# Optimization experiments

Measured on AMD Instinct MI355X. Metric: run time of the kernel, lower is better.

The kernel has to match this reference:

```python
import jax, jax.numpy as jnp
import numpy as np

N = 50000   # num nodes
E = 800000  # num edges
D = 128     # in_features
C = 1.0     # curvature c
MIN_NORM = 1e-15
BALL_EPS = 4e-3  # float32 boundary eps in PoincareBall.proj


def setup_inputs() -> dict:
    key = jax.random.key(0)
    k1, k2 = jax.random.split(key)
    x = jax.random.normal(k1, (N, D), dtype=jnp.float32)
    edge_index = jax.random.randint(k2, (2, E), 0, N, dtype=jnp.int32)
    return {"x": x, "edge_index": edge_index}


def _expmap0(u, c):
    sqrt_c = c ** 0.5
    u_norm = jnp.maximum(jnp.linalg.norm(u, axis=-1, keepdims=True), MIN_NORM)
    return jnp.tanh(sqrt_c * u_norm) * u / (sqrt_c * u_norm)


def _proj(p, c):
    norm = jnp.maximum(jnp.linalg.norm(p, axis=-1, keepdims=True), MIN_NORM)
    maxnorm = (1.0 - BALL_EPS) / (c ** 0.5)
    return jnp.where(norm > maxnorm, p / norm * maxnorm, p)


def reference(x, edge_index):
    row, col = edge_index[0], edge_index[1]
    # add_remaining_self_loops: drop existing self-loops (weight->0), append N fresh self-loops w=1
    w = jnp.where(row == col, 0.0, 1.0).astype(x.dtype)
    loop = jnp.arange(N, dtype=row.dtype)
    row_f = jnp.concatenate([row, loop])
    col_f = jnp.concatenate([col, loop])
    w_f = jnp.concatenate([w, jnp.ones((N,), x.dtype)])
    # symmetric GCN normalization: D^{-1/2} A D^{-1/2}
    deg = jax.ops.segment_sum(w_f, row_f, num_segments=N)
    dis = jnp.where(deg > 0, 1.0 / jnp.sqrt(jnp.where(deg > 0, deg, 1.0)), 0.0)
    nw = dis[row_f] * w_f * dis[col_f]  # [E+N]
    # gather source features, weighted scatter-add into destination rows
    support = nw[:, None] * x[col_f]                       # [E+N, D]
    result = jax.ops.segment_sum(support, row_f, num_segments=N)  # [N, D]
    return _proj(_expmap0(result, C), C)
```

## Files before the change

### kernel.cpp

```cpp
#include <hip/hip_runtime.h>
#include <math.h>

#define N_NODES 50000
#define N_EDGES 800000
#define DFEAT   128
#define MAXNORM (1.0f - 4e-3f)
#define CAP     64
#define OVF_CAP 8192


__global__ void k_zero(int* __restrict__ deg, int* __restrict__ ovf_cnt, int n) {
    int i = blockIdx.x * blockDim.x + threadIdx.x;
    if (i < n) deg[i] = 0;
    if (i == 0) *ovf_cnt = 0;
}

__global__ void k_build(const int* __restrict__ row, const int* __restrict__ col,
                        int* __restrict__ deg, int* __restrict__ adj,
                        int* __restrict__ ovf, int* __restrict__ ovf_cnt, int e) {
    int i = blockIdx.x * blockDim.x + threadIdx.x;
    if (i >= e) return;
    int r = row[i], c = col[i];
    if (r != c) {
        int pos = atomicAdd(&deg[r], 1);
        if (pos < CAP) adj[r * CAP + pos] = c;
        else {
            int o = atomicAdd(ovf_cnt, 1);
            if (o < OVF_CAP) { ovf[2 * o] = r; ovf[2 * o + 1] = c; }
        }
    }
}

__global__ __launch_bounds__(256) void k_prep(const float* __restrict__ x,
                                              const int* __restrict__ deg,
                                              unsigned int* __restrict__ xb,
                                              int nthreads) {
    int t = blockIdx.x * blockDim.x + threadIdx.x;
    if (t >= nthreads) return;

    int node = t >> 4;
    int part = t & 15;
    unsigned int w[4];
    if (node < N_NODES) {
        float dis = rsqrtf((float)(deg[node] + 1));
        const float4* x4 = (const float4*)(x + (size_t)node * DFEAT + part * 8);
        float4 a = x4[0];
        float4 b = x4[1];
        float fs[8] = {a.x, a.y, a.z, a.w, b.x, b.y, b.z, b.w};
        #pragma unroll
        for (int k = 0; k < 4; ++k) {
            unsigned int lo = __float_as_uint(fs[2 * k] * dis);
            unsigned int hi = __float_as_uint(fs[2 * k + 1] * dis);
            lo = (lo + 0x7FFFu + ((lo >> 16) & 1u)) >> 16;
            hi = (hi + 0x7FFFu + ((hi >> 16) & 1u)) >> 16;
            w[k] = lo | (hi << 16);
        }
    } else {
        w[0] = w[1] = w[2] = w[3] = 0u;
    }
    ((uint4*)xb)[t] = make_uint4(w[0], w[1], w[2], w[3]);
}

__device__ __forceinline__ float bf_lo(unsigned int w) { return __uint_as_float(w << 16); }
__device__ __forceinline__ float bf_hi(unsigned int w) { return __uint_as_float(w & 0xFFFF0000u); }

__global__ __launch_bounds__(256) void k_gather_bf(const unsigned int* __restrict__ xb,
                                                   const int* __restrict__ adj,
                                                   const int* __restrict__ deg,
                                                   const int* __restrict__ ovf,
                                                   const int* __restrict__ ovf_cnt,
                                                   float* __restrict__ out, int n) {
    int lane = threadIdx.x & 63;
    int half = lane >> 5;
    int fl   = lane & 31;
    int rowi = blockIdx.x * 4 + (threadIdx.x >> 6);
    if (rowi >= n) return;

    int cnt    = deg[rowi];
    int capcnt = cnt < CAP ? cnt : CAP;
    int capR   = (capcnt + 7) & ~7;

    int a = N_NODES;
    if (lane < capcnt) a = adj[rowi * CAP + lane];

    const unsigned int* __restrict__ xw = xb + 2 * fl;

    float acc0 = 0.f, acc1 = 0.f, acc2 = 0.f, acc3 = 0.f;
    for (int nb = 0; nb < capR; nb += 8) {
        int c0 = __shfl(a, nb + 0 + half);
        int c1 = __shfl(a, nb + 2 + half);
        int c2 = __shfl(a, nb + 4 + half);
        int c3 = __shfl(a, nb + 6 + half);
        uint2 v0 = *(const uint2*)(xw + c0 * (DFEAT / 2));
        uint2 v1 = *(const uint2*)(xw + c1 * (DFEAT / 2));
        uint2 v2 = *(const uint2*)(xw + c2 * (DFEAT / 2));
        uint2 v3 = *(const uint2*)(xw + c3 * (DFEAT / 2));
        acc0 += bf_lo(v0.x); acc1 += bf_hi(v0.x); acc2 += bf_lo(v0.y); acc3 += bf_hi(v0.y);
        acc0 += bf_lo(v1.x); acc1 += bf_hi(v1.x); acc2 += bf_lo(v1.y); acc3 += bf_hi(v1.y);
        acc0 += bf_lo(v2.x); acc1 += bf_hi(v2.x); acc2 += bf_lo(v2.y); acc3 += bf_hi(v2.y);
        acc0 += bf_lo(v3.x); acc1 += bf_hi(v3.x); acc2 += bf_lo(v3.y); acc3 += bf_hi(v3.y);
    }

    int novf = *ovf_cnt;
    if (novf > 0 && half == 0) {
        for (int k = 0; k < novf; ++k) {
            if (ovf[2 * k] == rowi) {
                uint2 v = *(const uint2*)(xw + ovf[2 * k + 1] * (DFEAT / 2));
                acc0 += bf_lo(v.x); acc1 += bf_hi(v.x);
                acc2 += bf_lo(v.y); acc3 += bf_hi(v.y);
            }
        }
    }

    acc0 += __shfl_xor(acc0, 32);
    acc1 += __shfl_xor(acc1, 32);
    acc2 += __shfl_xor(acc2, 32);
    acc3 += __shfl_xor(acc3, 32);

    uint2 sv = *(const uint2*)(xw + rowi * (DFEAT / 2));
    acc0 += bf_lo(sv.x); acc1 += bf_hi(sv.x);
    acc2 += bf_lo(sv.y); acc3 += bf_hi(sv.y);

    float di = rsqrtf((float)(cnt + 1));
    acc0 *= di; acc1 *= di; acc2 *= di; acc3 *= di;

    float nsq = acc0 * acc0 + acc1 * acc1 + acc2 * acc2 + acc3 * acc3;
    #pragma unroll
    for (int off = 16; off > 0; off >>= 1) nsq += __shfl_xor(nsq, off);

    float un = fmaxf(sqrtf(nsq), 1e-15f);
    float th = tanhf(un);
    float scale = th / un;
    if (th > MAXNORM) scale *= MAXNORM / th;

    if (half == 0) {
        float4 o = make_float4(acc0 * scale, acc1 * scale, acc2 * scale, acc3 * scale);
        *(float4*)(out + (size_t)rowi * DFEAT + 4 * fl) = o;
    }
}


__global__ __launch_bounds__(256) void k_gather_pad(const float* __restrict__ x,
                                                    const int* __restrict__ adj,
                                                    const int* __restrict__ deg,
                                                    const int* __restrict__ ovf,
                                                    const int* __restrict__ ovf_cnt,
                                                    float* __restrict__ out, int n) {
    int lane = threadIdx.x & 63;
    int rowi = blockIdx.x * 4 + (threadIdx.x >> 6);
    if (rowi >= n) return;

    const float2* __restrict__ x2 = (const float2*)x;
    int cnt    = deg[rowi];
    int capcnt = cnt < CAP ? cnt : CAP;

    int a = 0;
    if (lane < capcnt) a = adj[rowi * CAP + lane];

    float2 acc = make_float2(0.0f, 0.0f);
    for (int nb = 0; nb < capcnt; ++nb) {
        int c = __shfl(a, nb);
        float w = rsqrtf((float)(deg[c] + 1));
        float2 v = x2[c * (DFEAT / 2) + lane];
        acc.x += w * v.x;
        acc.y += w * v.y;
    }

    int novf = *ovf_cnt;
    for (int k = 0; k < novf; ++k) {
        if (ovf[2 * k] == rowi) {
            int c = ovf[2 * k + 1];
            float w = rsqrtf((float)(deg[c] + 1));
            float2 v = x2[c * (DFEAT / 2) + lane];
            acc.x += w * v.x;
            acc.y += w * v.y;
        }
    }

    float di = rsqrtf((float)(cnt + 1));
    float2 self = x2[rowi * (DFEAT / 2) + lane];
    acc.x = di * (acc.x + di * self.x);
    acc.y = di * (acc.y + di * self.y);

    float nsq = acc.x * acc.x + acc.y * acc.y;
    #pragma unroll
    for (int off = 32; off > 0; off >>= 1) nsq += __shfl_xor(nsq, off);

    float un = fmaxf(sqrtf(nsq), 1e-15f);
    float th = tanhf(un);
    float scale = th / un;
    if (th > MAXNORM) scale *= MAXNORM / th;

    float2 o = make_float2(acc.x * scale, acc.y * scale);
    ((float2*)out)[rowi * (DFEAT / 2) + lane] = o;
}


#define SCAN_BLK 256
#define NUM_SCAN_BLOCKS ((N_NODES + SCAN_BLK - 1) / SCAN_BLK)

__global__ void k_init_deg(int* __restrict__ deg, int n) {
    int i = blockIdx.x * blockDim.x + threadIdx.x;
    if (i < n) deg[i] = 1;
}

__global__ void k_hist(const int* __restrict__ row, const int* __restrict__ col,
                       int* __restrict__ deg, int e) {
    int i = blockIdx.x * blockDim.x + threadIdx.x;
    if (i < e) {
        int r = row[i], c = col[i];
        if (r != c) atomicAdd(&deg[r], 1);
    }
}

__global__ __launch_bounds__(SCAN_BLK) void k_block_sums(const int* __restrict__ deg,
                                                         int* __restrict__ blockSums, int n) {
    __shared__ int s[SCAN_BLK];
    int t = threadIdx.x;
    int i = blockIdx.x * SCAN_BLK + t;
    s[t] = (i < n) ? (deg[i] - 1) : 0;
    __syncthreads();
    for (int off = SCAN_BLK / 2; off > 0; off >>= 1) {
        if (t < off) s[t] += s[t + off];
        __syncthreads();
    }
    if (t == 0) blockSums[blockIdx.x] = s[0];
}

__global__ __launch_bounds__(SCAN_BLK) void k_scan_blocks(const int* __restrict__ blockSums,
                                                          int* __restrict__ blockBase) {
    __shared__ int s[SCAN_BLK];
    int t = threadIdx.x;
    s[t] = (t < NUM_SCAN_BLOCKS) ? blockSums[t] : 0;
    __syncthreads();
    for (int off = 1; off < SCAN_BLK; off <<= 1) {
        int v = (t >= off) ? s[t - off] : 0;
        __syncthreads();
        s[t] += v;
        __syncthreads();
    }
    if (t < NUM_SCAN_BLOCKS) blockBase[t] = (t == 0) ? 0 : s[t - 1];
}

__global__ __launch_bounds__(SCAN_BLK) void k_block_scan(const int* __restrict__ deg,
                                                         const int* __restrict__ blockBase,
                                                         int* __restrict__ offs,
                                                         int* __restrict__ cursor, int n) {
    __shared__ int s[SCAN_BLK];
    int t = threadIdx.x;
    int i = blockIdx.x * SCAN_BLK + t;
    int cnt = (i < n) ? (deg[i] - 1) : 0;
    s[t] = cnt;
    __syncthreads();
    for (int off = 1; off < SCAN_BLK; off <<= 1) {
        int v = (t >= off) ? s[t - off] : 0;
        __syncthreads();
        s[t] += v;
        __syncthreads();
    }
    if (i < n) {
        int excl = s[t] - cnt + blockBase[blockIdx.x];
        offs[i]   = excl;
        cursor[i] = excl;
    }
}

__global__ void k_scatter(const int* __restrict__ row, const int* __restrict__ col,
                          int* __restrict__ cursor, int* __restrict__ adj, int e) {
    int i = blockIdx.x * blockDim.x + threadIdx.x;
    if (i < e) {
        int r = row[i], c = col[i];
        if (r != c) {
            int pos = atomicAdd(&cursor[r], 1);
            adj[pos] = c;
        }
    }
}

__global__ __launch_bounds__(256) void k_gather_csr(const float* __restrict__ x,
                                                    const int* __restrict__ adj,
                                                    const int* __restrict__ offs,
                                                    const int* __restrict__ deg,
                                                    float* __restrict__ out, int n) {
    int lane = threadIdx.x & 63;
    int rowi = blockIdx.x * 4 + (threadIdx.x >> 6);
    if (rowi >= n) return;

    const float2* __restrict__ x2 = (const float2*)x;
    int beg = offs[rowi];
    int cnt = deg[rowi] - 1;

    float2 acc = make_float2(0.0f, 0.0f);
    for (int base = 0; base < cnt; base += 64) {
        int m = cnt - base; if (m > 64) m = 64;
        int a = 0;
        if (lane < m) a = adj[beg + base + lane];
        for (int nb = 0; nb < m; ++nb) {
            int c = __shfl(a, nb);
            float w = rsqrtf((float)deg[c]);
            float2 v = x2[c * (DFEAT / 2) + lane];
            acc.x += w * v.x;
            acc.y += w * v.y;
        }
    }
    float di = rsqrtf((float)deg[rowi]);
    float2 self = x2[rowi * (DFEAT / 2) + lane];
    acc.x = di * (acc.x + di * self.x);
    acc.y = di * (acc.y + di * self.y);

    float nsq = acc.x * acc.x + acc.y * acc.y;
    #pragma unroll
    for (int off = 32; off > 0; off >>= 1) nsq += __shfl_xor(nsq, off);

    float un = fmaxf(sqrtf(nsq), 1e-15f);
    float th = tanhf(un);
    float scale = th / un;
    if (th > MAXNORM) scale *= MAXNORM / th;

    float2 o = make_float2(acc.x * scale, acc.y * scale);
    ((float2*)out)[rowi * (DFEAT / 2) + lane] = o;
}


extern "C" void kernel_launch(void* const* d_in, const int* in_sizes, int n_in,
                              void* d_out, int out_size, void* d_ws, size_t ws_size,
                              hipStream_t stream) {
    const float* x          = (const float*)d_in[0];
    const int*   edge_index = (const int*)d_in[1];
    const int*   row = edge_index;
    const int*   col = edge_index + N_EDGES;
    float* out = (float*)d_out;
    char*  ws  = (char*)d_ws;

    size_t sz_xb  = sizeof(unsigned short) * (size_t)(N_NODES + 1) * DFEAT;
    size_t sz_adj = sizeof(int) * (size_t)N_NODES * CAP;
    size_t sz_deg = sizeof(int) * (size_t)N_NODES;
    size_t need_bf  = sz_xb + sz_adj + sz_deg + sizeof(int) * (1 + 2 * (size_t)OVF_CAP);
    size_t need_pad = sz_adj + sz_deg + sizeof(int) * (1 + 2 * (size_t)OVF_CAP);

    dim3 blk(256);
    if (ws_size >= need_bf) {
        size_t off = 0;
        unsigned int* xb = (unsigned int*)(ws + off); off += sz_xb;
        int* adj     = (int*)(ws + off); off += sz_adj;
        int* deg     = (int*)(ws + off); off += sz_deg;
        int* ovf_cnt = (int*)(ws + off); off += sizeof(int);
        int* ovf     = (int*)(ws + off);

        int nprep = (N_NODES + 1) * (DFEAT / 8);
        k_zero<<<dim3((N_NODES + 255) / 256), blk, 0, stream>>>(deg, ovf_cnt, N_NODES);
        k_build<<<dim3((N_EDGES + 255) / 256), blk, 0, stream>>>(row, col, deg, adj, ovf, ovf_cnt, N_EDGES);
        k_prep<<<dim3((nprep + 255) / 256), blk, 0, stream>>>(x, deg, xb, nprep);
        k_gather_bf<<<dim3((N_NODES + 3) / 4), blk, 0, stream>>>(xb, adj, deg, ovf, ovf_cnt, out, N_NODES);
    } else if (ws_size >= need_pad) {
        size_t off = 0;
        int* adj     = (int*)(ws + off); off += sz_adj;
        int* deg     = (int*)(ws + off); off += sz_deg;
        int* ovf_cnt = (int*)(ws + off); off += sizeof(int);
        int* ovf     = (int*)(ws + off);

        k_zero<<<dim3((N_NODES + 255) / 256), blk, 0, stream>>>(deg, ovf_cnt, N_NODES);
        k_build<<<dim3((N_EDGES + 255) / 256), blk, 0, stream>>>(row, col, deg, adj, ovf, ovf_cnt, N_EDGES);
        k_gather_pad<<<dim3((N_NODES + 3) / 4), blk, 0, stream>>>(x, adj, deg, ovf, ovf_cnt, out, N_NODES);
    } else {
        size_t off = 0;
        int* deg       = (int*)(ws + off); off += sizeof(int) * (size_t)N_NODES;
        int* offs      = (int*)(ws + off); off += sizeof(int) * (size_t)N_NODES;
        int* cursor    = (int*)(ws + off); off += sizeof(int) * (size_t)N_NODES;
        int* blockSums = (int*)(ws + off); off += sizeof(int) * (size_t)NUM_SCAN_BLOCKS;
        int* blockBase = (int*)(ws + off); off += sizeof(int) * (size_t)NUM_SCAN_BLOCKS;
        int* adj       = (int*)(ws + off);

        k_init_deg<<<dim3((N_NODES + 255) / 256), blk, 0, stream>>>(deg, N_NODES);
        k_hist<<<dim3((N_EDGES + 255) / 256), blk, 0, stream>>>(row, col, deg, N_EDGES);
        k_block_sums<<<dim3(NUM_SCAN_BLOCKS), dim3(SCAN_BLK), 0, stream>>>(deg, blockSums, N_NODES);
        k_scan_blocks<<<dim3(1), dim3(SCAN_BLK), 0, stream>>>(blockSums, blockBase);
        k_block_scan<<<dim3(NUM_SCAN_BLOCKS), dim3(SCAN_BLK), 0, stream>>>(deg, blockBase, offs, cursor, N_NODES);
        k_scatter<<<dim3((N_EDGES + 255) / 256), blk, 0, stream>>>(row, col, cursor, adj, N_EDGES);
        k_gather_csr<<<dim3((N_NODES + 3) / 4), blk, 0, stream>>>(x, adj, offs, deg, out, N_NODES);
    }
}
```

Measured before the change: 160.1 us.

## Build adjacency via node buckets and LDS, store 16-bit neighbor ids

Edges are first binned into 512 global buckets of 98 destination nodes, each edge packed as (row<<16|col). A per-bucket block then builds per-node degrees and a sentinel-padded 16-bit adjacency list in shared memory, writes both out with coalesced stores, and converts and scales its nodes' features to bf16. This fuses the former prep kernel into the build and halves adjacency traffic for the gather. The aim is to replace scattered global atomics and stores with LDS work. The cost is heavy atomic contention on only 512 bucket counters, and degrees would be wrong if a bucket exceeds 2048 edges. The padded fp32 fallback path is removed.

```diff
diff --git a/kernel.cpp b/kernel.cpp
--- a/kernel.cpp
+++ b/kernel.cpp
@@ -7,65 +7,106 @@
 #define MAXNORM (1.0f - 4e-3f)
 #define CAP     64
 #define OVF_CAP 8192
-
-
-__global__ void k_zero(int* __restrict__ deg, int* __restrict__ ovf_cnt, int n) {
-    int i = blockIdx.x * blockDim.x + threadIdx.x;
-    if (i < n) deg[i] = 0;
-    if (i == 0) *ovf_cnt = 0;
-}
-
-__global__ void k_build(const int* __restrict__ row, const int* __restrict__ col,
-                        int* __restrict__ deg, int* __restrict__ adj,
-                        int* __restrict__ ovf, int* __restrict__ ovf_cnt, int e) {
+#define NB      512
+#define NPB     98
+#define BKT_CAP 2048
+#define SENT    N_NODES
+
+
+__global__ void k_zero(int* __restrict__ bcnt, int* __restrict__ ovf_cnt) {
+    int i = blockIdx.x * blockDim.x + threadIdx.x;
+    if (i < NB) bcnt[i] = 0;
+    if (i == NB) *ovf_cnt = 0;
+}
+
+__global__ void k_bin(const int* __restrict__ row, const int* __restrict__ col,
+                      int* __restrict__ bcnt, unsigned int* __restrict__ bucket,
+                      int* __restrict__ ovf, int* __restrict__ ovf_cnt, int e) {
     int i = blockIdx.x * blockDim.x + threadIdx.x;
     if (i >= e) return;
     int r = row[i], c = col[i];
-    if (r != c) {
-        int pos = atomicAdd(&deg[r], 1);
-        if (pos < CAP) adj[r * CAP + pos] = c;
+    if (r == c) return;
+    int b = r / NPB;
+    int pos = atomicAdd(&bcnt[b], 1);
+    if (pos < BKT_CAP) bucket[b * BKT_CAP + pos] = ((unsigned int)r << 16) | (unsigned int)c;
+    else {
+        int o = atomicAdd(ovf_cnt, 1);
+        if (o < OVF_CAP) { ovf[2 * o] = r; ovf[2 * o + 1] = c; }
+    }
+}
+
+__device__ __forceinline__ unsigned int pack_bf16(float lo_f, float hi_f) {
+    unsigned int lo = __float_as_uint(lo_f);
+    unsigned int hi = __float_as_uint(hi_f);
+    lo = (lo + 0x7FFFu + ((lo >> 16) & 1u)) >> 16;
+    hi = (hi + 0x7FFFu + ((hi >> 16) & 1u)) >> 16;
+    return lo | (hi << 16);
+}
+
+__global__ __launch_bounds__(256) void k_bucket(const float* __restrict__ x,
+                                                const unsigned int* __restrict__ bucket,
+                                                const int* __restrict__ bcnt,
+                                                int* __restrict__ deg,
+                                                unsigned short* __restrict__ adj16,
+                                                unsigned int* __restrict__ xb,
+                                                int* __restrict__ ovf, int* __restrict__ ovf_cnt) {
+    __shared__ int ldeg[NPB];
+    __shared__ __align__(16) unsigned short ladj[NPB * CAP];
+    unsigned int* ladj32 = (unsigned int*)ladj;
+
+    int b = blockIdx.x;
+    int t = threadIdx.x;
+    int nbase = b * NPB;
+
+    for (int j = t; j < NPB; j += 256) ldeg[j] = 0;
+    for (int j = t; j < NPB * CAP / 2; j += 256) ladj32[j] = (((unsigned)SENT) << 16) | (unsigned)SENT;
+    __syncthreads();
+
+    int cnt = bcnt[b];
+    if (cnt > BKT_CAP) cnt = BKT_CAP;
+    for (int j = t; j < cnt; j += 256) {
+        unsigned int e = bucket[b * BKT_CAP + j];
+        int r = (int)(e >> 16), c = (int)(e & 0xFFFFu);
+        int lr = r - nbase;
+        int pos = atomicAdd(&ldeg[lr], 1);
+        if (pos < CAP) ladj[lr * CAP + pos] = (unsigned short)c;
         else {
             int o = atomicAdd(ovf_cnt, 1);
             if (o < OVF_CAP) { ovf[2 * o] = r; ovf[2 * o + 1] = c; }
         }
     }
-}
-
-__global__ __launch_bounds__(256) void k_prep(const float* __restrict__ x,
-                                              const int* __restrict__ deg,
-                                              unsigned int* __restrict__ xb,
-                                              int nthreads) {
-    int t = blockIdx.x * blockDim.x + threadIdx.x;
-    if (t >= nthreads) return;
-
-    int node = t >> 4;
-    int part = t & 15;
-    unsigned int w[4];
-    if (node < N_NODES) {
-        float dis = rsqrtf((float)(deg[node] + 1));
-        const float4* x4 = (const float4*)(x + (size_t)node * DFEAT + part * 8);
-        float4 a = x4[0];
-        float4 b = x4[1];
-        float fs[8] = {a.x, a.y, a.z, a.w, b.x, b.y, b.z, b.w};
-        #pragma unroll
-        for (int k = 0; k < 4; ++k) {
-            unsigned int lo = __float_as_uint(fs[2 * k] * dis);
-            unsigned int hi = __float_as_uint(fs[2 * k + 1] * dis);
-            lo = (lo + 0x7FFFu + ((lo >> 16) & 1u)) >> 16;
-            hi = (hi + 0x7FFFu + ((hi >> 16) & 1u)) >> 16;
-            w[k] = lo | (hi << 16);
-        }
-    } else {
-        w[0] = w[1] = w[2] = w[3] = 0u;
-    }
-    ((uint4*)xb)[t] = make_uint4(w[0], w[1], w[2], w[3]);
+    __syncthreads();
+
+    int nclip = N_NODES - nbase;
+    if (nclip > NPB) nclip = NPB;
+    if (nclip > 0) {
+        if (t < nclip) deg[nbase + t] = ldeg[t];
+        unsigned int* gadj = (unsigned int*)(adj16 + (size_t)nbase * CAP);
+        int nw = nclip * (CAP / 2);
+        for (int j = t; j < nw; j += 256) gadj[j] = ladj32[j];
+        const float4* gx = (const float4*)(x + (size_t)nbase * DFEAT);
+        uint2* gxb = (uint2*)xb;
+        int nf4 = nclip * 32;
+        for (int j = t; j < nf4; j += 256) {
+            int node = j >> 5;
+            float dis = rsqrtf((float)(ldeg[node] + 1));
+            float4 v = gx[j];
+            uint2 o;
+            o.x = pack_bf16(v.x * dis, v.y * dis);
+            o.y = pack_bf16(v.z * dis, v.w * dis);
+            gxb[(size_t)(nbase + node) * 32 + (j & 31)] = o;
+        }
+    }
+    if (b == NB - 1) {
+        for (int j = t; j < DFEAT / 2; j += 256) xb[(size_t)N_NODES * (DFEAT / 2) + j] = 0u;
+    }
 }
 
 __device__ __forceinline__ float bf_lo(unsigned int w) { return __uint_as_float(w << 16); }
 __device__ __forceinline__ float bf_hi(unsigned int w) { return __uint_as_float(w & 0xFFFF0000u); }
 
 __global__ __launch_bounds__(256) void k_gather_bf(const unsigned int* __restrict__ xb,
-                                                   const int* __restrict__ adj,
+                                                   const unsigned short* __restrict__ adj16,
                                                    const int* __restrict__ deg,
                                                    const int* __restrict__ ovf,
                                                    const int* __restrict__ ovf_cnt,
@@ -80,8 +121,7 @@
     int capcnt = cnt < CAP ? cnt : CAP;
     int capR   = (capcnt + 7) & ~7;
 
-    int a = N_NODES;
-    if (lane < capcnt) a = adj[rowi * CAP + lane];
+    int a = (int)adj16[rowi * CAP + lane];
 
     const unsigned int* __restrict__ xw = xb + 2 * fl;
 
@@ -140,62 +180,6 @@
 }
 
 
-__global__ __launch_bounds__(256) void k_gather_pad(const float* __restrict__ x,
-                                                    const int* __restrict__ adj,
-                                                    const int* __restrict__ deg,
-                                                    const int* __restrict__ ovf,
-                                                    const int* __restrict__ ovf_cnt,
-                                                    float* __restrict__ out, int n) {
-    int lane = threadIdx.x & 63;
-    int rowi = blockIdx.x * 4 + (threadIdx.x >> 6);
-    if (rowi >= n) return;
-
-    const float2* __restrict__ x2 = (const float2*)x;
-    int cnt    = deg[rowi];
-    int capcnt = cnt < CAP ? cnt : CAP;
-
-    int a = 0;
-    if (lane < capcnt) a = adj[rowi * CAP + lane];
-
-    float2 acc = make_float2(0.0f, 0.0f);
-    for (int nb = 0; nb < capcnt; ++nb) {
-        int c = __shfl(a, nb);
-        float w = rsqrtf((float)(deg[c] + 1));
-        float2 v = x2[c * (DFEAT / 2) + lane];
-        acc.x += w * v.x;
-        acc.y += w * v.y;
-    }
-
-    int novf = *ovf_cnt;
-    for (int k = 0; k < novf; ++k) {
-        if (ovf[2 * k] == rowi) {
-            int c = ovf[2 * k + 1];
-            float w = rsqrtf((float)(deg[c] + 1));
-            float2 v = x2[c * (DFEAT / 2) + lane];
-            acc.x += w * v.x;
-            acc.y += w * v.y;
-        }
-    }
-
-    float di = rsqrtf((float)(cnt + 1));
-    float2 self = x2[rowi * (DFEAT / 2) + lane];
-    acc.x = di * (acc.x + di * self.x);
-    acc.y = di * (acc.y + di * self.y);
-
-    float nsq = acc.x * acc.x + acc.y * acc.y;
-    #pragma unroll
-    for (int off = 32; off > 0; off >>= 1) nsq += __shfl_xor(nsq, off);
-
-    float un = fmaxf(sqrtf(nsq), 1e-15f);
-    float th = tanhf(un);
-    float scale = th / un;
-    if (th > MAXNORM) scale *= MAXNORM / th;
-
-    float2 o = make_float2(acc.x * scale, acc.y * scale);
-    ((float2*)out)[rowi * (DFEAT / 2) + lane] = o;
-}
-
-
 #define SCAN_BLK 256
 #define NUM_SCAN_BLOCKS ((N_NODES + SCAN_BLK - 1) / SCAN_BLK)
 
@@ -332,36 +316,29 @@
     float* out = (float*)d_out;
     char*  ws  = (char*)d_ws;
 
-    size_t sz_xb  = sizeof(unsigned short) * (size_t)(N_NODES + 1) * DFEAT;
-    size_t sz_adj = sizeof(int) * (size_t)N_NODES * CAP;
-    size_t sz_deg = sizeof(int) * (size_t)N_NODES;
-    size_t need_bf  = sz_xb + sz_adj + sz_deg + sizeof(int) * (1 + 2 * (size_t)OVF_CAP);
-    size_t need_pad = sz_adj + sz_deg + sizeof(int) * (1 + 2 * (size_t)OVF_CAP);
+    size_t sz_xb     = sizeof(unsigned short) * (size_t)(N_NODES + 1) * DFEAT;
+    size_t sz_bucket = sizeof(unsigned int) * (size_t)NB * BKT_CAP;
+    size_t sz_adj16  = sizeof(unsigned short) * (size_t)N_NODES * CAP;
+    size_t sz_deg    = sizeof(int) * (size_t)N_NODES;
+    size_t sz_bcnt   = sizeof(int) * (size_t)NB;
+    size_t need = sz_xb + sz_bucket + sz_adj16 + sz_deg + sz_bcnt
+                + sizeof(int) * (1 + 2 * (size_t)OVF_CAP);
 
     dim3 blk(256);
-    if (ws_size >= need_bf) {
+    if (ws_size >= need) {
         size_t off = 0;
-        unsigned int* xb = (unsigned int*)(ws + off); off += sz_xb;
-        int* adj     = (int*)(ws + off); off += sz_adj;
-        int* deg     = (int*)(ws + off); off += sz_deg;
-        int* ovf_cnt = (int*)(ws + off); off += sizeof(int);
-        int* ovf     = (int*)(ws + off);
-
-        int nprep = (N_NODES + 1) * (DFEAT / 8);
-        k_zero<<<dim3((N_NODES + 255) / 256), blk, 0, stream>>>(deg, ovf_cnt, N_NODES);
-        k_build<<<dim3((N_EDGES + 255) / 256), blk, 0, stream>>>(row, col, deg, adj, ovf, ovf_cnt, N_EDGES);
-        k_prep<<<dim3((nprep + 255) / 256), blk, 0, stream>>>(x, deg, xb, nprep);
-        k_gather_bf<<<dim3((N_NODES + 3) / 4), blk, 0, stream>>>(xb, adj, deg, ovf, ovf_cnt, out, N_NODES);
-    } else if (ws_size >= need_pad) {
-        size_t off = 0;
-        int* adj     = (int*)(ws + off); off += sz_adj;
-        int* deg     = (int*)(ws + off); off += sz_deg;
-        int* ovf_cnt = (int*)(ws + off); off += sizeof(int);
-        int* ovf     = (int*)(ws + off);
-
-        k_zero<<<dim3((N_NODES + 255) / 256), blk, 0, stream>>>(deg, ovf_cnt, N_NODES);
-        k_build<<<dim3((N_EDGES + 255) / 256), blk, 0, stream>>>(row, col, deg, adj, ovf, ovf_cnt, N_EDGES);
-        k_gather_pad<<<dim3((N_NODES + 3) / 4), blk, 0, stream>>>(x, adj, deg, ovf, ovf_cnt, out, N_NODES);
+        unsigned int*   xb     = (unsigned int*)(ws + off);   off += sz_xb;
+        unsigned int*   bucket = (unsigned int*)(ws + off);   off += sz_bucket;
+        unsigned short* adj16  = (unsigned short*)(ws + off); off += sz_adj16;
+        int*            deg    = (int*)(ws + off);            off += sz_deg;
+        int*            bcnt   = (int*)(ws + off);            off += sz_bcnt;
+        int*            ovf_cnt= (int*)(ws + off);            off += sizeof(int);
+        int*            ovf    = (int*)(ws + off);
+
+        k_zero<<<dim3((NB + 1 + 255) / 256), blk, 0, stream>>>(bcnt, ovf_cnt);
+        k_bin<<<dim3((N_EDGES + 255) / 256), blk, 0, stream>>>(row, col, bcnt, bucket, ovf, ovf_cnt, N_EDGES);
+        k_bucket<<<dim3(NB), blk, 0, stream>>>(x, bucket, bcnt, deg, adj16, xb, ovf, ovf_cnt);
+        k_gather_bf<<<dim3((N_NODES + 3) / 4), blk, 0, stream>>>(xb, adj16, deg, ovf, ovf_cnt, out, N_NODES);
     } else {
         size_t off = 0;
         int* deg       = (int*)(ws + off); off += sizeof(int) * (size_t)N_NODES;
```

Measured after the change: 361.6 us. 126% more time.

## Partition adjacency build by destination range and store neighbor ids as 16-bit

Applied to the files above, without the earlier changes.

The build kernel now launches 8192 blocks split into 8 destination-row partitions. Each partition scans all edges but only inserts those whose row falls in its range, so atomics and adjacency writes stay in a smaller region of memory. Adjacency entries are stored as unsigned short instead of int, halving the adjacency footprint for the build writes and the gather reads. The padded fp32 fallback path is removed. Storing node ids in 16 bits is only safe if ids fit, but N=50000 fits, while the edge list is now read eight times.

```diff
diff --git a/kernel.cpp b/kernel.cpp
--- a/kernel.cpp
+++ b/kernel.cpp
@@ -7,6 +7,9 @@
 #define MAXNORM (1.0f - 4e-3f)
 #define CAP     64
 #define OVF_CAP 8192
+#define NPART   8
+#define PSIZE   (N_NODES / NPART)
+#define SENT    N_NODES
 
 
 __global__ void k_zero(int* __restrict__ deg, int* __restrict__ ovf_cnt, int n) {
@@ -16,14 +19,17 @@
 }
 
 __global__ void k_build(const int* __restrict__ row, const int* __restrict__ col,
-                        int* __restrict__ deg, int* __restrict__ adj,
+                        int* __restrict__ deg, unsigned short* __restrict__ adj16,
                         int* __restrict__ ovf, int* __restrict__ ovf_cnt, int e) {
-    int i = blockIdx.x * blockDim.x + threadIdx.x;
-    if (i >= e) return;
-    int r = row[i], c = col[i];
-    if (r != c) {
+    int p      = blockIdx.x & (NPART - 1);
+    int vblock = blockIdx.x >> 3;
+    int stride = (gridDim.x >> 3) * blockDim.x;
+    int lo = p * PSIZE, hi = lo + PSIZE;
+    for (int i = vblock * blockDim.x + threadIdx.x; i < e; i += stride) {
+        int r = row[i], c = col[i];
+        if (r < lo || r >= hi || r == c) continue;
         int pos = atomicAdd(&deg[r], 1);
-        if (pos < CAP) adj[r * CAP + pos] = c;
+        if (pos < CAP) adj16[r * CAP + pos] = (unsigned short)c;
         else {
             int o = atomicAdd(ovf_cnt, 1);
             if (o < OVF_CAP) { ovf[2 * o] = r; ovf[2 * o + 1] = c; }
@@ -65,7 +71,7 @@
 __device__ __forceinline__ float bf_hi(unsigned int w) { return __uint_as_float(w & 0xFFFF0000u); }
 
 __global__ __launch_bounds__(256) void k_gather_bf(const unsigned int* __restrict__ xb,
-                                                   const int* __restrict__ adj,
+                                                   const unsigned short* __restrict__ adj16,
                                                    const int* __restrict__ deg,
                                                    const int* __restrict__ ovf,
                                                    const int* __restrict__ ovf_cnt,
@@ -80,8 +86,8 @@
     int capcnt = cnt < CAP ? cnt : CAP;
     int capR   = (capcnt + 7) & ~7;
 
-    int a = N_NODES;
-    if (lane < capcnt) a = adj[rowi * CAP + lane];
+    int a = SENT;
+    if (lane < capcnt) a = (int)adj16[rowi * CAP + lane];
 
     const unsigned int* __restrict__ xw = xb + 2 * fl;
 
@@ -140,62 +146,6 @@
 }
 
 
-__global__ __launch_bounds__(256) void k_gather_pad(const float* __restrict__ x,
-                                                    const int* __restrict__ adj,
-                                                    const int* __restrict__ deg,
-                                                    const int* __restrict__ ovf,
-                                                    const int* __restrict__ ovf_cnt,
-                                                    float* __restrict__ out, int n) {
-    int lane = threadIdx.x & 63;
-    int rowi = blockIdx.x * 4 + (threadIdx.x >> 6);
-    if (rowi >= n) return;
-
-    const float2* __restrict__ x2 = (const float2*)x;
-    int cnt    = deg[rowi];
-    int capcnt = cnt < CAP ? cnt : CAP;
-
-    int a = 0;
-    if (lane < capcnt) a = adj[rowi * CAP + lane];
-
-    float2 acc = make_float2(0.0f, 0.0f);
-    for (int nb = 0; nb < capcnt; ++nb) {
-        int c = __shfl(a, nb);
-        float w = rsqrtf((float)(deg[c] + 1));
-        float2 v = x2[c * (DFEAT / 2) + lane];
-        acc.x += w * v.x;
-        acc.y += w * v.y;
-    }
-
-    int novf = *ovf_cnt;
-    for (int k = 0; k < novf; ++k) {
-        if (ovf[2 * k] == rowi) {
-            int c = ovf[2 * k + 1];
-            float w = rsqrtf((float)(deg[c] + 1));
-            float2 v = x2[c * (DFEAT / 2) + lane];
-            acc.x += w * v.x;
-            acc.y += w * v.y;
-        }
-    }
-
-    float di = rsqrtf((float)(cnt + 1));
-    float2 self = x2[rowi * (DFEAT / 2) + lane];
-    acc.x = di * (acc.x + di * self.x);
-    acc.y = di * (acc.y + di * self.y);
-
-    float nsq = acc.x * acc.x + acc.y * acc.y;
-    #pragma unroll
-    for (int off = 32; off > 0; off >>= 1) nsq += __shfl_xor(nsq, off);
-
-    float un = fmaxf(sqrtf(nsq), 1e-15f);
-    float th = tanhf(un);
-    float scale = th / un;
-    if (th > MAXNORM) scale *= MAXNORM / th;
-
-    float2 o = make_float2(acc.x * scale, acc.y * scale);
-    ((float2*)out)[rowi * (DFEAT / 2) + lane] = o;
-}
-
-
 #define SCAN_BLK 256
 #define NUM_SCAN_BLOCKS ((N_NODES + SCAN_BLK - 1) / SCAN_BLK)
 
@@ -332,36 +282,25 @@
     float* out = (float*)d_out;
     char*  ws  = (char*)d_ws;
 
-    size_t sz_xb  = sizeof(unsigned short) * (size_t)(N_NODES + 1) * DFEAT;
-    size_t sz_adj = sizeof(int) * (size_t)N_NODES * CAP;
-    size_t sz_deg = sizeof(int) * (size_t)N_NODES;
-    size_t need_bf  = sz_xb + sz_adj + sz_deg + sizeof(int) * (1 + 2 * (size_t)OVF_CAP);
-    size_t need_pad = sz_adj + sz_deg + sizeof(int) * (1 + 2 * (size_t)OVF_CAP);
+    size_t sz_xb    = sizeof(unsigned short) * (size_t)(N_NODES + 1) * DFEAT;
+    size_t sz_adj16 = sizeof(unsigned short) * (size_t)N_NODES * CAP;
+    size_t sz_deg   = sizeof(int) * (size_t)N_NODES;
+    size_t need = sz_xb + sz_adj16 + sz_deg + sizeof(int) * (1 + 2 * (size_t)OVF_CAP);
 
     dim3 blk(256);
-    if (ws_size >= need_bf) {
+    if (ws_size >= need) {
         size_t off = 0;
-        unsigned int* xb = (unsigned int*)(ws + off); off += sz_xb;
-        int* adj     = (int*)(ws + off); off += sz_adj;
-        int* deg     = (int*)(ws + off); off += sz_deg;
-        int* ovf_cnt = (int*)(ws + off); off += sizeof(int);
-        int* ovf     = (int*)(ws + off);
+        unsigned int*   xb      = (unsigned int*)(ws + off);   off += sz_xb;
+        unsigned short* adj16   = (unsigned short*)(ws + off); off += sz_adj16;
+        int*            deg     = (int*)(ws + off);            off += sz_deg;
+        int*            ovf_cnt = (int*)(ws + off);            off += sizeof(int);
+        int*            ovf     = (int*)(ws + off);
 
         int nprep = (N_NODES + 1) * (DFEAT / 8);
         k_zero<<<dim3((N_NODES + 255) / 256), blk, 0, stream>>>(deg, ovf_cnt, N_NODES);
-        k_build<<<dim3((N_EDGES + 255) / 256), blk, 0, stream>>>(row, col, deg, adj, ovf, ovf_cnt, N_EDGES);
+        k_build<<<dim3(8192), blk, 0, stream>>>(row, col, deg, adj16, ovf, ovf_cnt, N_EDGES);
         k_prep<<<dim3((nprep + 255) / 256), blk, 0, stream>>>(x, deg, xb, nprep);
-        k_gather_bf<<<dim3((N_NODES + 3) / 4), blk, 0, stream>>>(xb, adj, deg, ovf, ovf_cnt, out, N_NODES);
-    } else if (ws_size >= need_pad) {
-        size_t off = 0;
-        int* adj     = (int*)(ws + off); off += sz_adj;
-        int* deg     = (int*)(ws + off); off += sz_deg;
-        int* ovf_cnt = (int*)(ws + off); off += sizeof(int);
-        int* ovf     = (int*)(ws + off);
-
-        k_zero<<<dim3((N_NODES + 255) / 256), blk, 0, stream>>>(deg, ovf_cnt, N_NODES);
-        k_build<<<dim3((N_EDGES + 255) / 256), blk, 0, stream>>>(row, col, deg, adj, ovf, ovf_cnt, N_EDGES);
-        k_gather_pad<<<dim3((N_NODES + 3) / 4), blk, 0, stream>>>(x, adj, deg, ovf, ovf_cnt, out, N_NODES);
+        k_gather_bf<<<dim3((N_NODES + 3) / 4), blk, 0, stream>>>(xb, adj16, deg, ovf, ovf_cnt, out, N_NODES);
     } else {
         size_t off = 0;
         int* deg       = (int*)(ws + off); off += sizeof(int) * (size_t)N_NODES;
```

New measurement: 148.6 us. 1.08x faster.
